# Performance work log

Measured on AMD Instinct MI355X. Metric: run time of the kernel, lower is better.

Reference implementation:

```python
import jax, jax.numpy as jnp
import numpy as np

B, S, D, H = 2, 2048, 1024, 16
DK = D // H


def setup_inputs() -> dict:
    key = jax.random.key(0)
    ks = jax.random.split(key, 8)
    query = jax.random.normal(ks[0], (B, S, D), dtype=jnp.float32)
    key_t = jax.random.normal(ks[1], (B, S, D), dtype=jnp.float32)
    value = jax.random.normal(ks[2], (B, S, D), dtype=jnp.float32)
    # causal mask (1 = attend, 0 = masked), broadcast over batch and heads
    mask = jnp.tril(jnp.ones((S, S), dtype=jnp.int32))[None, None, :, :]
    scale = 1.0 / np.sqrt(D)
    w_q = jax.random.normal(ks[3], (D, D), dtype=jnp.float32) * scale
    w_k = jax.random.normal(ks[4], (D, D), dtype=jnp.float32) * scale
    w_v = jax.random.normal(ks[5], (D, D), dtype=jnp.float32) * scale
    w_o = jax.random.normal(ks[6], (D, D), dtype=jnp.float32) * scale
    b_o = jnp.zeros((D,), dtype=jnp.float32)
    return {"query": query, "key": key_t, "value": value, "mask": mask,
            "w_q": w_q, "w_k": w_k, "w_v": w_v, "w_o": w_o, "b_o": b_o}


def reference(query, key, value, mask, w_q, w_k, w_v, w_o, b_o):
    # projections: nn.Linear applies x @ W.T; weights here stored as [out, in]
    def proj(x, w):  # [B,S,D] -> [B,H,S,DK]
        y = jnp.einsum('bsd,ed->bse', x, w)
        return y.reshape(B, S, H, DK).transpose(0, 2, 1, 3)

    Q = proj(query, w_q)
    K = proj(key, w_k)
    V = proj(value, w_v)

    scores = jnp.einsum('bhqd,bhkd->bhqk', Q, K) / jnp.sqrt(jnp.float32(DK))
    scores = jnp.where(mask == 0, jnp.float32(-1e9), scores)
    attention_weights = jax.nn.softmax(scores, axis=-1)  # dropout p=0 (eval)
    context = jnp.einsum('bhqk,bhkd->bhqd', attention_weights, V)
    context = context.transpose(0, 2, 1, 3).reshape(B, S, D)
    output = jnp.einsum('bsd,ed->bse', context, w_o) + b_o
    return output, attention_weights
```

## Files before the change

kernel.cpp:

```cpp
#include <hip/hip_runtime.h>
#include <hip/hip_bf16.h>
#include <math.h>

#define B_  2
#define S_  2048
#define D_  1024
#define H_  16
#define DK_ 64

typedef __attribute__((ext_vector_type(8))) short bf16x8;
typedef __attribute__((ext_vector_type(4))) float f32x4;
typedef __attribute__((ext_vector_type(8))) unsigned short u16x8;
typedef __attribute__((ext_vector_type(4))) unsigned short u16x4;

#define MFMA16(a, b, c) __builtin_amdgcn_mfma_f32_16x16x32_bf16((a), (b), (c), 0, 0, 0)

__device__ __forceinline__ unsigned short f2bf(float f) {
    union { float f; unsigned u; } v; v.f = f;
    unsigned r = v.u + 0x7fffu + ((v.u >> 16) & 1u);
    return (unsigned short)(r >> 16);
}
__device__ __forceinline__ float bf2f(unsigned short u) {
    return __uint_as_float(((unsigned)u) << 16);
}

__global__ __launch_bounds__(256) void cvt_all(
        const float* __restrict__ q, const float* __restrict__ k, const float* __restrict__ v,
        const float* __restrict__ wq, const float* __restrict__ wk,
        const float* __restrict__ wv, const float* __restrict__ wo,
        unsigned short* __restrict__ xq, unsigned short* __restrict__ xk,
        unsigned short* __restrict__ xv, unsigned short* __restrict__ wqb,
        unsigned short* __restrict__ wkb, unsigned short* __restrict__ wvb,
        unsigned short* __restrict__ wob) {
    int i = blockIdx.x * 256 + threadIdx.x;
    const float* src; unsigned short* dst; int off;
    if      (i < 1048576) { src = q;  dst = xq;  off = 0; }
    else if (i < 2097152) { src = k;  dst = xk;  off = 1048576; }
    else if (i < 3145728) { src = v;  dst = xv;  off = 2097152; }
    else if (i < 3407872) { src = wq; dst = wqb; off = 3145728; }
    else if (i < 3670016) { src = wk; dst = wkb; off = 3407872; }
    else if (i < 3932160) { src = wv; dst = wvb; off = 3670016; }
    else                  { src = wo; dst = wob; off = 3932160; }
    i -= off;
    float4 f = reinterpret_cast<const float4*>(src)[i];
    ushort4 o;
    o.x = f2bf(f.x); o.y = f2bf(f.y); o.z = f2bf(f.z); o.w = f2bf(f.w);
    reinterpret_cast<ushort4*>(dst)[i] = o;
}

__global__ __launch_bounds__(256) void gemm_bt(const unsigned short* __restrict__ A,
                                               const unsigned short* __restrict__ W,
                                               void* __restrict__ out,
                                               const float* __restrict__ bias,
                                               int mode, float scale) {
    __shared__ char eplds[4 * 9216];
    const int lane = threadIdx.x & 63;
    const int row  = lane & 15, quad = lane >> 4;
    const int w    = threadIdx.x >> 6;
    const int wid  = blockIdx.x * 4 + w;
    const int m0   = (wid & 127) * 32;
    const int n0   = (wid >> 7) * 64;
    f32x4 acc[2][4] = {};
    const unsigned short* Ap = A + (m0 + row) * D_ + quad * 8;
    const unsigned short* Wp = W + (n0 + row) * D_ + quad * 8;
    for (int k0 = 0; k0 < D_; k0 += 32) {
        bf16x8 a0 = *(const bf16x8*)(Ap + k0);
        bf16x8 a1 = *(const bf16x8*)(Ap + 16 * D_ + k0);
        bf16x8 w0 = *(const bf16x8*)(Wp + k0);
        bf16x8 w1 = *(const bf16x8*)(Wp + 16 * D_ + k0);
        bf16x8 w2 = *(const bf16x8*)(Wp + 32 * D_ + k0);
        bf16x8 w3 = *(const bf16x8*)(Wp + 48 * D_ + k0);
        acc[0][0] = MFMA16(a0, w0, acc[0][0]);
        acc[0][1] = MFMA16(a0, w1, acc[0][1]);
        acc[0][2] = MFMA16(a0, w2, acc[0][2]);
        acc[0][3] = MFMA16(a0, w3, acc[0][3]);
        acc[1][0] = MFMA16(a1, w0, acc[1][0]);
        acc[1][1] = MFMA16(a1, w1, acc[1][1]);
        acc[1][2] = MFMA16(a1, w2, acc[1][2]);
        acc[1][3] = MFMA16(a1, w3, acc[1][3]);
    }
    char* myep = eplds + w * 9216;
    const int b = m0 >> 11;
    const int h = n0 >> 6;
    if (mode == 0) {
        unsigned short* lt = (unsigned short*)myep;
#pragma unroll
        for (int mi = 0; mi < 2; mi++)
#pragma unroll
            for (int t = 0; t < 4; t++)
#pragma unroll
                for (int r = 0; r < 4; r++)
                    lt[(mi * 16 + quad * 4 + r) * 72 + t * 16 + row] = f2bf(acc[mi][t][r] * scale);
        __builtin_amdgcn_sched_barrier(0);
        unsigned short* Qout = (unsigned short*)out;
#pragma unroll
        for (int pass = 0; pass < 4; pass++) {
            int rr = pass * 8 + (lane >> 3);
            int cc = (lane & 7) * 8;
            u16x8 val = *(const u16x8*)(lt + rr * 72 + cc);
            int s = (m0 + rr) & (S_ - 1);
            *(u16x8*)(&Qout[(((size_t)(b * H_ + h)) * S_ + s) * DK_ + cc]) = val;
        }
    } else if (mode == 1) {
        unsigned short* lt = (unsigned short*)myep;
#pragma unroll
        for (int mi = 0; mi < 2; mi++)
#pragma unroll
            for (int t = 0; t < 4; t++)
#pragma unroll
                for (int r = 0; r < 4; r++)
                    lt[(t * 16 + row) * 40 + mi * 16 + quad * 4 + r] = f2bf(acc[mi][t][r]);
        __builtin_amdgcn_sched_barrier(0);
        unsigned short* Vout = (unsigned short*)out;
#pragma unroll
        for (int pass = 0; pass < 8; pass++) {
            int dk = pass * 8 + (lane >> 3);
            int so = (lane & 7) * 4;
            u16x4 val = *(const u16x4*)(lt + dk * 40 + so);
            *(u16x4*)(&Vout[(((size_t)(b * H_ + h)) * DK_ + dk) * S_ + (m0 & (S_ - 1)) + so]) = val;
        }
    } else {
        float* lt32 = (float*)myep;
        float bs[4];
#pragma unroll
        for (int t = 0; t < 4; t++) bs[t] = bias[n0 + t * 16 + row];
#pragma unroll
        for (int mi = 0; mi < 2; mi++)
#pragma unroll
            for (int t = 0; t < 4; t++)
#pragma unroll
                for (int r = 0; r < 4; r++)
                    lt32[(mi * 16 + quad * 4 + r) * 72 + t * 16 + row] = acc[mi][t][r] + bs[t];
        __builtin_amdgcn_sched_barrier(0);
        float* outF = (float*)out;
#pragma unroll
        for (int pass = 0; pass < 8; pass++) {
            int rr = pass * 4 + (lane >> 4);
            int cc = (lane & 15) * 4;
            float4 val = *(const float4*)(lt32 + rr * 72 + cc);
            *(float4*)(&outF[(size_t)(m0 + rr) * D_ + n0 + cc]) = val;
        }
    }
}

__global__ __launch_bounds__(256) void attn_kernel(const unsigned short* __restrict__ Qb,
                                                   const unsigned short* __restrict__ Kb,
                                                   const unsigned short* __restrict__ Vt,
                                                   float* __restrict__ Pbase,
                                                   unsigned short* __restrict__ ctx) {
    __shared__ unsigned short plds[4][16 * 40];
    __shared__ float olds[4][16 * 64];
    __shared__ float llds[4][16];
    const int w    = threadIdx.x >> 6;
    const int lane = threadIdx.x & 63;
    const int row  = lane & 15, quad = lane >> 4;
    const int tile = 127 - (int)(blockIdx.x >> 5);
    const int bh   = blockIdx.x & 31;
    const int q0   = tile * 16;
    const int b    = bh >> 4, h = bh & 15;
    const unsigned short* Qh = Qb + (size_t)bh * S_ * DK_;
    const unsigned short* Kh = Kb + (size_t)bh * S_ * DK_;
    const unsigned short* Vh = Vt + (size_t)bh * DK_ * S_;
    float* P = Pbase + (size_t)bh * S_ * S_;

    bf16x8 aq0 = *(const bf16x8*)(Qh + (q0 + row) * DK_ + quad * 8);
    bf16x8 aq1 = *(const bf16x8*)(Qh + (q0 + row) * DK_ + 32 + quad * 8);

    const int nks   = (q0 + 47) >> 5;
    const int nfull = (q0 + 1) >> 5;

    float l_l[4] = {0.f, 0.f, 0.f, 0.f};
    for (int ks = w; ks < nks; ks += 4) {
        const int c0k = ks * 32;
        const bool diag = (ks >= nfull);
#pragma unroll
        for (int half = 0; half < 2; half++) {
            const int c = c0k + half * 16;
            const unsigned short* kp = Kh + (c + row) * DK_ + quad * 8;
            bf16x8 k0 = *(const bf16x8*)kp;
            bf16x8 k1 = *(const bf16x8*)(kp + 32);
            f32x4 sa = {};
            sa = MFMA16(aq0, k0, sa);
            sa = MFMA16(aq1, k1, sa);
#pragma unroll
            for (int r = 0; r < 4; r++) {
                float p = __expf(sa[r]);
                if (diag) p = ((c + row) <= (q0 + quad * 4 + r)) ? p : 0.f;
                l_l[r] += p;
            }
        }
    }
#pragma unroll
    for (int r = 0; r < 4; r++) {
#pragma unroll
        for (int off = 1; off < 16; off <<= 1)
            l_l[r] += __shfl_xor(l_l[r], off, 16);
        if (row == 0) llds[w][quad * 4 + r] = l_l[r];
    }
    __syncthreads();
    float invL[4];
#pragma unroll
    for (int r = 0; r < 4; r++)
        invL[r] = 1.0f / (llds[0][quad * 4 + r] + llds[1][quad * 4 + r] +
                          llds[2][quad * 4 + r] + llds[3][quad * 4 + r]);

    f32x4 o[4] = {};
    unsigned short* myld = plds[w];
    for (int ks = w; ks < nks; ks += 4) {
        const int c0k = ks * 32;
        const bool diag = (ks >= nfull);
#pragma unroll
        for (int half = 0; half < 2; half++) {
            const int c = c0k + half * 16;
            const unsigned short* kp = Kh + (c + row) * DK_ + quad * 8;
            bf16x8 k0 = *(const bf16x8*)kp;
            bf16x8 k1 = *(const bf16x8*)(kp + 32);
            f32x4 sa = {};
            sa = MFMA16(aq0, k0, sa);
            sa = MFMA16(aq1, k1, sa);
#pragma unroll
            for (int r = 0; r < 4; r++) {
                float p = __expf(sa[r]) * invL[r];
                if (diag) p = ((c + row) <= (q0 + quad * 4 + r)) ? p : 0.f;
                myld[(quad * 4 + r) * 40 + half * 16 + row] = f2bf(p);
            }
        }
        __builtin_amdgcn_sched_barrier(0);
#pragma unroll
        for (int g = 0; g < 2; g++) {
            int rr = g * 8 + (lane >> 3);
            int cg = (lane & 7) * 4;
            u16x4 pb = *(const u16x4*)(myld + rr * 40 + cg);
            float4 pv;
            pv.x = bf2f((unsigned short)pb[0]);
            pv.y = bf2f((unsigned short)pb[1]);
            pv.z = bf2f((unsigned short)pb[2]);
            pv.w = bf2f((unsigned short)pb[3]);
            *(float4*)(&P[(size_t)(q0 + rr) * S_ + c0k + cg]) = pv;
        }
        bf16x8 pf = *(const bf16x8*)(myld + row * 40 + quad * 8);
#pragma unroll
        for (int t4 = 0; t4 < 4; t4++) {
            bf16x8 vv = *(const bf16x8*)(Vh + (t4 * 16 + row) * S_ + c0k + quad * 8);
            o[t4] = MFMA16(pf, vv, o[t4]);
        }
        __builtin_amdgcn_sched_barrier(0);
    }

    float* myo = olds[w];
#pragma unroll
    for (int t4 = 0; t4 < 4; t4++)
#pragma unroll
        for (int r = 0; r < 4; r++)
            myo[(quad * 4 + r) * 64 + t4 * 16 + row] = o[t4][r];
    __syncthreads();
    {
        int i  = threadIdx.x;
        int rr = i >> 4, c4 = (i & 15) * 4;
        u16x4 cv;
#pragma unroll
        for (int j = 0; j < 4; j++) {
            float s = olds[0][rr * 64 + c4 + j] + olds[1][rr * 64 + c4 + j] +
                      olds[2][rr * 64 + c4 + j] + olds[3][rr * 64 + c4 + j];
            cv[j] = (short)f2bf(s);
        }
        *(u16x4*)(&ctx[((size_t)(b * S_) + q0 + rr) * D_ + h * DK_ + c4]) = cv;
    }

    const int cb = nks * 32;
    if (cb < S_) {
        const int nq = (S_ - cb) >> 2;
        for (int i = threadIdx.x; i < 16 * nq; i += 256) {
            int rr = i / nq, cc = i - rr * nq;
            *reinterpret_cast<float4*>(&P[(size_t)(q0 + rr) * S_ + cb + cc * 4]) =
                make_float4(0.f, 0.f, 0.f, 0.f);
        }
    }
}

extern "C" void kernel_launch(void* const* d_in, const int* in_sizes, int n_in,
                              void* d_out, int out_size, void* d_ws, size_t ws_size,
                              hipStream_t stream) {
    const float* q  = (const float*)d_in[0];
    const float* k  = (const float*)d_in[1];
    const float* v  = (const float*)d_in[2];
    const float* wq = (const float*)d_in[4];
    const float* wk = (const float*)d_in[5];
    const float* wv = (const float*)d_in[6];
    const float* wo = (const float*)d_in[7];
    const float* bo = (const float*)d_in[8];

    unsigned short* ws  = (unsigned short*)d_ws;
    unsigned short* xq  = ws;
    unsigned short* xk  = ws + 4194304;
    unsigned short* xv  = ws + 8388608;
    unsigned short* wqb = ws + 12582912;
    unsigned short* wkb = wqb + 1048576;
    unsigned short* wvb = wkb + 1048576;
    unsigned short* wob = wvb + 1048576;
    unsigned short* Qb  = ws + 16777216;
    unsigned short* Kb  = Qb + 4194304;
    unsigned short* Vt  = Kb + 4194304;
    unsigned short* ctx = Vt + 4194304;
    float* outp  = (float*)d_out;
    float* Pbase = outp + 4194304;

    cvt_all<<<16384, 256, 0, stream>>>(q, k, v, wq, wk, wv, wo,
                                       xq, xk, xv, wqb, wkb, wvb, wob);

    gemm_bt<<<512, 256, 0, stream>>>(xq, wqb, Qb, nullptr, 0, 0.125f);
    gemm_bt<<<512, 256, 0, stream>>>(xk, wkb, Kb, nullptr, 0, 1.0f);
    gemm_bt<<<512, 256, 0, stream>>>(xv, wvb, Vt, nullptr, 1, 1.0f);

    attn_kernel<<<4096, 256, 0, stream>>>(Qb, Kb, Vt, Pbase, ctx);

    gemm_bt<<<512, 256, 0, stream>>>(ctx, wob, outp, bo, 2, 1.0f);
}
```

Baseline: 910.2 us.

## Merge QKV projection launches and use nontemporal loads/stores for streaming data

```diff
diff --git a/kernel.cpp b/kernel.cpp
--- a/kernel.cpp
+++ b/kernel.cpp
@@ -42,22 +42,19 @@
     else if (i < 3932160) { src = wv; dst = wvb; off = 3670016; }
     else                  { src = wo; dst = wob; off = 3932160; }
     i -= off;
-    float4 f = reinterpret_cast<const float4*>(src)[i];
+    f32x4 f = __builtin_nontemporal_load(reinterpret_cast<const f32x4*>(src) + i);
     ushort4 o;
-    o.x = f2bf(f.x); o.y = f2bf(f.y); o.z = f2bf(f.z); o.w = f2bf(f.w);
+    o.x = f2bf(f[0]); o.y = f2bf(f[1]); o.z = f2bf(f[2]); o.w = f2bf(f[3]);
     reinterpret_cast<ushort4*>(dst)[i] = o;
 }
 
-__global__ __launch_bounds__(256) void gemm_bt(const unsigned short* __restrict__ A,
-                                               const unsigned short* __restrict__ W,
-                                               void* __restrict__ out,
-                                               const float* __restrict__ bias,
-                                               int mode, float scale) {
-    __shared__ char eplds[4 * 9216];
+__device__ __forceinline__ void gemm_bt_body(char* myep, int blk,
+        const unsigned short* __restrict__ A, const unsigned short* __restrict__ W,
+        void* __restrict__ out, const float* __restrict__ bias, int mode, float scale) {
     const int lane = threadIdx.x & 63;
     const int row  = lane & 15, quad = lane >> 4;
     const int w    = threadIdx.x >> 6;
-    const int wid  = blockIdx.x * 4 + w;
+    const int wid  = blk * 4 + w;
     const int m0   = (wid & 127) * 32;
     const int n0   = (wid >> 7) * 64;
     f32x4 acc[2][4] = {};
@@ -79,7 +76,6 @@
         acc[1][2] = MFMA16(a1, w2, acc[1][2]);
         acc[1][3] = MFMA16(a1, w3, acc[1][3]);
     }
-    char* myep = eplds + w * 9216;
     const int b = m0 >> 11;
     const int h = n0 >> 6;
     if (mode == 0) {
@@ -137,10 +133,32 @@
         for (int pass = 0; pass < 8; pass++) {
             int rr = pass * 4 + (lane >> 4);
             int cc = (lane & 15) * 4;
-            float4 val = *(const float4*)(lt32 + rr * 72 + cc);
-            *(float4*)(&outF[(size_t)(m0 + rr) * D_ + n0 + cc]) = val;
-        }
-    }
+            f32x4 val = *(const f32x4*)(lt32 + rr * 72 + cc);
+            __builtin_nontemporal_store(val, (f32x4*)(&outF[(size_t)(m0 + rr) * D_ + n0 + cc]));
+        }
+    }
+}
+
+__global__ __launch_bounds__(256) void gemm_qkv(
+        const unsigned short* __restrict__ xq, const unsigned short* __restrict__ xk,
+        const unsigned short* __restrict__ xv, const unsigned short* __restrict__ wqb,
+        const unsigned short* __restrict__ wkb, const unsigned short* __restrict__ wvb,
+        unsigned short* __restrict__ Qb, unsigned short* __restrict__ Kb,
+        unsigned short* __restrict__ Vt) {
+    __shared__ char eplds[4 * 5120];
+    char* myep = eplds + (threadIdx.x >> 6) * 5120;
+    const int which = blockIdx.x >> 9;
+    const int blk   = blockIdx.x & 511;
+    if (which == 0)      gemm_bt_body(myep, blk, xq, wqb, Qb, nullptr, 0, 0.125f);
+    else if (which == 1) gemm_bt_body(myep, blk, xk, wkb, Kb, nullptr, 0, 1.0f);
+    else                 gemm_bt_body(myep, blk, xv, wvb, Vt, nullptr, 1, 1.0f);
+}
+
+__global__ __launch_bounds__(256) void gemm_out(
+        const unsigned short* __restrict__ A, const unsigned short* __restrict__ W,
+        float* __restrict__ out, const float* __restrict__ bias) {
+    __shared__ char eplds[4 * 9216];
+    gemm_bt_body(eplds + (threadIdx.x >> 6) * 9216, blockIdx.x, A, W, out, bias, 2, 1.0f);
 }
 
 __global__ __launch_bounds__(256) void attn_kernel(const unsigned short* __restrict__ Qb,
@@ -231,12 +249,12 @@
             int rr = g * 8 + (lane >> 3);
             int cg = (lane & 7) * 4;
             u16x4 pb = *(const u16x4*)(myld + rr * 40 + cg);
-            float4 pv;
-            pv.x = bf2f((unsigned short)pb[0]);
-            pv.y = bf2f((unsigned short)pb[1]);
-            pv.z = bf2f((unsigned short)pb[2]);
-            pv.w = bf2f((unsigned short)pb[3]);
-            *(float4*)(&P[(size_t)(q0 + rr) * S_ + c0k + cg]) = pv;
+            f32x4 pv;
+            pv[0] = bf2f((unsigned short)pb[0]);
+            pv[1] = bf2f((unsigned short)pb[1]);
+            pv[2] = bf2f((unsigned short)pb[2]);
+            pv[3] = bf2f((unsigned short)pb[3]);
+            __builtin_nontemporal_store(pv, (f32x4*)(&P[(size_t)(q0 + rr) * S_ + c0k + cg]));
         }
         bf16x8 pf = *(const bf16x8*)(myld + row * 40 + quad * 8);
 #pragma unroll
@@ -270,10 +288,11 @@
     const int cb = nks * 32;
     if (cb < S_) {
         const int nq = (S_ - cb) >> 2;
+        const f32x4 z = {0.f, 0.f, 0.f, 0.f};
         for (int i = threadIdx.x; i < 16 * nq; i += 256) {
             int rr = i / nq, cc = i - rr * nq;
-            *reinterpret_cast<float4*>(&P[(size_t)(q0 + rr) * S_ + cb + cc * 4]) =
-                make_float4(0.f, 0.f, 0.f, 0.f);
+            __builtin_nontemporal_store(z,
+                reinterpret_cast<f32x4*>(&P[(size_t)(q0 + rr) * S_ + cb + cc * 4]));
         }
     }
 }
@@ -308,11 +327,9 @@
     cvt_all<<<16384, 256, 0, stream>>>(q, k, v, wq, wk, wv, wo,
                                        xq, xk, xv, wqb, wkb, wvb, wob);
 
-    gemm_bt<<<512, 256, 0, stream>>>(xq, wqb, Qb, nullptr, 0, 0.125f);
-    gemm_bt<<<512, 256, 0, stream>>>(xk, wkb, Kb, nullptr, 0, 1.0f);
-    gemm_bt<<<512, 256, 0, stream>>>(xv, wvb, Vt, nullptr, 1, 1.0f);
+    gemm_qkv<<<1536, 256, 0, stream>>>(xq, xk, xv, wqb, wkb, wvb, Qb, Kb, Vt);
 
     attn_kernel<<<4096, 256, 0, stream>>>(Qb, Kb, Vt, Pbase, ctx);
 
-    gemm_bt<<<512, 256, 0, stream>>>(ctx, wob, outp, bo, 2, 1.0f);
-}
+    gemm_out<<<512, 256, 0, stream>>>(ctx, wob, outp, bo);
+}
```

Measured after the change: 884.8 us. -2.8%, faster.
